# Performance work log

Hardware: AMD Instinct MI355X
Metric: run time of the kernel (lower is better)

## Reference

```python
import jax, jax.numpy as jnp
import numpy as np

B, LD = 256, 64
NO, LO = 10240, 32
NM, LM = 81920, 16
EO, EM = 81920, 327680
E, HID, H, Dh, V = 128, 256, 8, 16, 10000


def masked_mean(tokens, table):
    # tokens: [N, L] int; pad id = 0
    emb = table[tokens]                            # [N, L, E]
    mask = (tokens != 0)
    s = jnp.sum(emb * mask[..., None].astype(emb.dtype), axis=1)
    lens = jnp.maximum(jnp.sum(mask, axis=1), 1).astype(emb.dtype)
    return s / lens[:, None]


def segment_softmax(scores, seg, num_segments):
    # scores: [E, ...]; softmax over entries sharing seg id (PyG softmax)
    m = jax.ops.segment_max(scores, seg, num_segments=num_segments)
    e = jnp.exp(scores - m[seg])
    s = jax.ops.segment_sum(e, seg, num_segments=num_segments)
    return e / (s[seg] + 1e-16)


def gcn_conv(x, W, b, src, dst, n):
    # PyG GCNConv: normalize=True, add_self_loops=True
    xw = x @ W
    loops = jnp.arange(n, dtype=src.dtype)
    s2 = jnp.concatenate([src, loops])
    d2 = jnp.concatenate([dst, loops])
    deg = jax.ops.segment_sum(jnp.ones_like(d2, dtype=x.dtype), d2, num_segments=n)
    dinv = deg ** -0.5  # deg >= 1 due to self loops
    norm = dinv[s2] * dinv[d2]
    out = jax.ops.segment_sum(xw[s2] * norm[:, None], d2, num_segments=n)
    return out + b


def transformer_conv(x, Wq, bq, Wk, bk, Wv, bv, Wskip, bskip, src, dst, n):
    q = (x @ Wq + bq).reshape(n, H, Dh)
    k = (x @ Wk + bk).reshape(n, H, Dh)
    v = (x @ Wv + bv).reshape(n, H, Dh)
    score = jnp.sum(q[dst] * k[src], axis=-1) / jnp.sqrt(jnp.asarray(Dh, x.dtype))  # [E, H]
    alpha = segment_softmax(score, dst, n)
    agg = jax.ops.segment_sum(alpha[:, :, None] * v[src], dst, num_segments=n)  # [n, H, Dh]
    return agg.reshape(n, H * Dh) + x @ Wskip + bskip


def global_attention(x, Wg, bg, seg, num_segments):
    gate = x @ Wg + bg                              # [N, 1]
    a = segment_softmax(gate, seg, num_segments)
    return jax.ops.segment_sum(a * x, seg, num_segments=num_segments)


def setup_inputs():
    key = jax.random.key(0)
    ks = jax.random.split(key, 20)
    sc = lambda k, shape: jax.random.normal(k, shape, dtype=jnp.float32) * 0.05
    inp = {
        "desc_tokens": jax.random.randint(ks[0], (B, LD), 0, V, dtype=jnp.int32),
        "x_tokens": jax.random.randint(ks[1], (NO, LO), 0, V, dtype=jnp.int32),
        "mini_tokens": jax.random.randint(ks[2], (NM, LM), 0, V, dtype=jnp.int32),
        "src": jax.random.randint(ks[3], (EO,), 0, NO, dtype=jnp.int32),
        "dst": jax.random.randint(ks[4], (EO,), 0, NO, dtype=jnp.int32),
        "mini_src": jax.random.randint(ks[5], (EM,), 0, NM, dtype=jnp.int32),
        "mini_dst": jax.random.randint(ks[6], (EM,), 0, NM, dtype=jnp.int32),
        "mini_batch": (jnp.arange(NM, dtype=jnp.int32) // (NM // NO)),
        "node_batch": (jnp.arange(NO, dtype=jnp.int32) // (NO // B)),
        "desc_table": sc(ks[7], (V, E)),
        "code_table": sc(ks[8], (V, E)),
        "code_table2": sc(ks[9], (V, E)),
        "Wq": sc(ks[10], (E, H * Dh)), "bq": jnp.zeros((H * Dh,), jnp.float32),
        "Wk": sc(ks[11], (E, H * Dh)), "bk": jnp.zeros((H * Dh,), jnp.float32),
        "Wv": sc(ks[12], (E, H * Dh)), "bv": jnp.zeros((H * Dh,), jnp.float32),
        "Wskip": sc(ks[13], (E, H * Dh)), "bskip": jnp.zeros((H * Dh,), jnp.float32),
        "W2": sc(ks[14], (E, HID)), "b2": jnp.zeros((HID,), jnp.float32),
        "W3": sc(ks[15], (HID, E)), "b3": jnp.zeros((E,), jnp.float32),
        "Wg": sc(ks[16], (E, 1)), "bg": jnp.zeros((1,), jnp.float32),
    }
    return inp


def reference(desc_tokens, x_tokens, mini_tokens, src, dst, mini_src, mini_dst,
              mini_batch, node_batch, desc_table, code_table, code_table2,
              Wq, bq, Wk, bk, Wv, bv, Wskip, bskip, W2, b2, W3, b3, Wg, bg):
    # encode_desc: embedding + masked mean pool -> [B, E]
    h_n = masked_mean(desc_tokens, desc_table)
    # encode_code_graph
    stmt_emb = masked_mean(x_tokens, code_table2)          # [NO, E]
    mini_emb = masked_mean(mini_tokens, code_table)        # [NM, E]
    mini_hidden = transformer_conv(mini_emb, Wq, bq, Wk, bk, Wv, bv,
                                   Wskip, bskip, mini_src, mini_dst, NM)
    mini_fn = global_attention(mini_hidden, Wg, bg, mini_batch, NO)  # [NO, E]
    mini_fn = (mini_fn + stmt_emb) * 0.5
    h = jax.nn.relu(gcn_conv(mini_fn, W2, b2, src, dst, NO))
    final_stmt = gcn_conv(h, W3, b3, src, dst, NO)
    fn_repr = global_attention(final_stmt, Wg, bg, node_batch, B)    # [B, E]
    # cosine similarity (torch eps=1e-8 clamps each norm)
    na = jnp.maximum(jnp.linalg.norm(fn_repr, axis=-1), 1e-8)
    nb = jnp.maximum(jnp.linalg.norm(h_n, axis=-1), 1e-8)
    return jnp.sum(fn_repr * h_n, axis=-1) / (na * nb)
```

## Files before the change

### kernel.cpp

```cpp
#include <hip/hip_runtime.h>
#include <hip/hip_bf16.h>
#include <math.h>

#define BB   256
#define LDE  64
#define NO   10240
#define LO   32
#define NM   81920
#define LM   16
#define EO   81920
#define EM   327680
#define ED   128
#define HIDD 256
#define NH   8
#define DH   16
#define VV   10000

static inline int nblk(long long n, int b) { return (int)((n + b - 1) / b); }

typedef __attribute__((ext_vector_type(8))) short short8;
typedef __attribute__((ext_vector_type(4))) float f32x4;

static __device__ __forceinline__ unsigned short bf16_rne(float f) {
  unsigned u = __float_as_uint(f);
  return (unsigned short)((u + 0x7fffu + ((u >> 16) & 1u)) >> 16);
}
static __device__ __forceinline__ float bf16_to_f(unsigned short h) {
  return __uint_as_float(((unsigned)h) << 16);
}
static __device__ __forceinline__ float4 b4f(ushort4 h) {
  return make_float4(bf16_to_f(h.x), bf16_to_f(h.y), bf16_to_f(h.z), bf16_to_f(h.w));
}
static __device__ __forceinline__ ushort4 f4b(float4 v) {
  return make_ushort4(bf16_rne(v.x), bf16_rne(v.y), bf16_rne(v.z), bf16_rne(v.w));
}

static __device__ __forceinline__ void gl_lds16(const void* g, void* l) {
  __builtin_amdgcn_global_load_lds(
      (const __attribute__((address_space(1))) unsigned int*)g,
      (__attribute__((address_space(3))) unsigned int*)l, 16, 0, 0);
}

struct ConvArgs {
  const float *Wq, *Wk, *Wv, *Ws, *W2, *W3;
  const float *bq, *bk, *bv, *bs;
  short8* frag;
  float* bias512;
  const float* t1; unsigned short* o1;
  const float* t2; unsigned short* o2;
  int* hist;
};
#define TBLK (2 * VV * ED / 4 / 256)
#define ZBLK ((NM + NO) / 256)
__global__ void __launch_bounds__(256)
conv_all_k(ConvArgs A) {
  int b = blockIdx.x;
  if (b < 32) {
    int g = b * 256 + threadIdx.x;
    int lane = g & 63, f = g >> 6;
    int jl = f & 7, kb = (f >> 3) & 3, ch = f >> 5;
    int cf = ch * 8 + jl;
    int c = cf * 16 + (lane & 15);
    int k0 = kb * 32 + ((lane >> 4) << 3);
    const float* wp; int cm;
    if (c < 128)      { wp = A.Wq; cm = c; }
    else if (c < 384) { int u = c - 128, t = u & 7;
                        wp = (t < 4) ? A.Wk : A.Wv; cm = (u >> 3) * 4 + (t & 3); }
    else              { wp = A.Ws; cm = c - 384; }
    short8 h;
    #pragma unroll
    for (int j = 0; j < 8; ++j)
      h[j] = (short)bf16_rne(wp[(size_t)(k0 + j) * 128 + cm]);
    A.frag[g] = h;
  } else if (b < 64) {
    int g = (b - 32) * 256 + threadIdx.x;
    const float* wp; int M, dstbase, gg;
    if (g < 4096) { wp = A.W2; M = 256; dstbase = 8192;  gg = g; }
    else          { wp = A.W3; M = 128; dstbase = 12288; gg = g - 4096; }
    int lane = gg & 63, fid = gg >> 6;
    int nt = fid % (M / 16), kb = fid / (M / 16);
    int n = nt * 16 + (lane & 15);
    int k0 = kb * 32 + ((lane >> 4) << 3);
    short8 h;
    #pragma unroll
    for (int j = 0; j < 8; ++j)
      h[j] = (short)bf16_rne(wp[(size_t)(k0 + j) * M + n]);
    A.frag[dstbase + gg] = h;
  } else if (b < 64 + TBLK) {
    int q = (b - 64) * 256 + threadIdx.x;
    const int NT = VV * ED / 4;
    if (q < NT) {
      float4 v = *(const float4*)(A.t1 + (size_t)q * 4);
      *(ushort4*)(A.o1 + (size_t)q * 4) = f4b(v);
    } else if (q < 2 * NT) {
      int q2 = q - NT;
      float4 v = *(const float4*)(A.t2 + (size_t)q2 * 4);
      *(ushort4*)(A.o2 + (size_t)q2 * 4) = f4b(v);
    }
  } else if (b < 64 + TBLK + ZBLK) {
    int i = (b - 64 - TBLK) * 256 + threadIdx.x;
    if (i < NM + NO) A.hist[i] = 0;
  } else {
    for (int c = threadIdx.x; c < 512; c += 256) {
      float v;
      if (c < 128)      v = A.bq[c];
      else if (c < 384) { int u = c - 128, t = u & 7;
                          v = (t < 4) ? A.bk[(u >> 3) * 4 + t] : A.bv[(u >> 3) * 4 + (t & 3)]; }
      else              v = A.bs[c - 384];
      A.bias512[c] = v;
    }
  }
}

template<int L>
static __device__ __forceinline__ void embed_body_f(const int* __restrict__ tokens,
                                                    const float* __restrict__ table,
                                                    float* __restrict__ out, int blk) {
  const int r = threadIdx.x >> 5, lane = threadIdx.x & 31;
  const int n0 = blk * 8;
  __shared__ int toks[8][L];
  for (int i = threadIdx.x; i < 8 * L; i += 256)
    toks[i / L][i % L] = tokens[(size_t)n0 * L + i];
  __syncthreads();
  float4 acc = make_float4(0.f, 0.f, 0.f, 0.f);
  int cnt = 0;
  #pragma unroll
  for (int l = 0; l < L; ++l) {
    int t = toks[r][l];
    float4 v = *(const float4*)(table + (size_t)t * ED + lane * 4);
    float msk = (t != 0) ? 1.f : 0.f;
    cnt += (t != 0);
    acc.x = fmaf(msk, v.x, acc.x); acc.y = fmaf(msk, v.y, acc.y);
    acc.z = fmaf(msk, v.z, acc.z); acc.w = fmaf(msk, v.w, acc.w);
  }
  float inv = 1.f / (float)(cnt > 0 ? cnt : 1);
  acc.x *= inv; acc.y *= inv; acc.z *= inv; acc.w *= inv;
  *(float4*)(out + (size_t)(n0 + r) * ED + lane * 4) = acc;
}

template<int L>
static __device__ __forceinline__ void embed_body16(const int* __restrict__ tokens,
                                                    const unsigned short* __restrict__ table,
                                                    unsigned short* __restrict__ out, int blk) {
  const int r = threadIdx.x >> 4, lane = threadIdx.x & 15;
  const int n0 = blk * 16;
  __shared__ int toks[16][L];
  for (int i = threadIdx.x; i < 16 * L; i += 256)
    toks[i / L][i % L] = tokens[(size_t)n0 * L + i];
  __syncthreads();
  float acc[8] = {};
  int cnt = 0;
  #pragma unroll
  for (int l = 0; l < L; ++l) {
    int t = toks[r][l];
    short8 v = *(const short8*)(table + (size_t)t * ED + lane * 8);
    float msk = (t != 0) ? 1.f : 0.f;
    cnt += (t != 0);
    #pragma unroll
    for (int j = 0; j < 8; ++j)
      acc[j] = fmaf(msk, bf16_to_f((unsigned short)v[j]), acc[j]);
  }
  float inv = 1.f / (float)(cnt > 0 ? cnt : 1);
  short8 o;
  #pragma unroll
  for (int j = 0; j < 8; ++j) o[j] = (short)bf16_rne(acc[j] * inv);
  *(short8*)(out + (size_t)(n0 + r) * ED + lane * 8) = o;
}

__global__ void __launch_bounds__(256)
embed_all_k(const int* __restrict__ desc_tokens, const float* __restrict__ desc_table,
            float* __restrict__ h_n,
            const int* __restrict__ x_tokens, const unsigned short* __restrict__ ctab2,
            unsigned short* __restrict__ stmt,
            const int* __restrict__ mini_tokens, const unsigned short* __restrict__ ctab,
            unsigned short* __restrict__ miniE) {
  int b = blockIdx.x;
  if (b < BB / 8) embed_body_f<LDE>(desc_tokens, desc_table, h_n, b);
  else if (b < BB / 8 + NO / 16) embed_body16<LO>(x_tokens, ctab2, stmt, b - BB / 8);
  else embed_body16<LM>(mini_tokens, ctab, miniE, b - BB / 8 - NO / 16);
}

__global__ void __launch_bounds__(512)
qkvs_merged_k(const unsigned short* __restrict__ Ab, const short8* __restrict__ Wf,
              const float* __restrict__ bias512, unsigned short* __restrict__ out) {
  const int id = blockIdx.x;
  const int blk = (id & 7) * 80 + (id >> 3);
  const int n0 = blk * 128;
  const int tid = threadIdx.x;
  const int w = tid >> 6, lane = tid & 63;
  const int r = lane & 15, qd = lane >> 4;
  const int node = n0 + w * 16 + r;
  __shared__ short8 wlds[2048];
  __shared__ short8 elds[8 * 144];
  char* myl = (char*)elds + w * 2304;

  short8 a[4];
  #pragma unroll
  for (int kb = 0; kb < 4; ++kb)
    a[kb] = *(const short8*)(Ab + (size_t)node * ED + kb * 32 + qd * 8);

  for (int ch = 0; ch < 4; ++ch) {
    {
      const char* gs = (const char*)Wf + (size_t)ch * 32768
                     + (size_t)(w * 4) * 1024 + (size_t)lane * 16;
      char* ls = (char*)wlds + (w * 4) * 1024;
      #pragma unroll
      for (int t = 0; t < 4; ++t)
        gl_lds16(gs + t * 1024, ls + t * 1024);
    }
    __syncthreads();

    #pragma unroll
    for (int hf = 0; hf < 2; ++hf) {
      #pragma unroll
      for (int j4 = 0; j4 < 4; ++j4) {
        const int jl = hf * 4 + j4;
        f32x4 acc = (f32x4){0.f, 0.f, 0.f, 0.f};
        #pragma unroll
        for (int kb = 0; kb < 4; ++kb) {
          short8 wf = *(const short8*)((const char*)wlds
                        + ((size_t)((kb << 3) | jl) * 64 + lane) * 16);
          acc = __builtin_amdgcn_mfma_f32_16x16x32_bf16(wf, a[kb], acc, 0, 0, 0);
        }
        const int cf = ch * 8 + jl;
        const float4 bv = *(const float4*)(bias512 + cf * 16 + qd * 4);
        ushort4 o;
        o.x = bf16_rne(acc[0] + bv.x);
        o.y = bf16_rne(acc[1] + bv.y);
        o.z = bf16_rne(acc[2] + bv.z);
        o.w = bf16_rne(acc[3] + bv.w);
        *(ushort4*)(myl + r * 144 + j4 * 32 + qd * 8) = o;
      }
      #pragma unroll
      for (int t = 0; t < 2; ++t) {
        const int rr = t * 8 + (lane >> 3);
        short8 v = *(const short8*)(myl + rr * 144 + (lane & 7) * 16);
        *(short8*)(out + (size_t)(n0 + w * 16 + rr) * 512
                   + ch * 128 + hf * 64 + (lane & 7) * 8) = v;
      }
    }
    __syncthreads();
  }
}

template<bool RELU>
__global__ void __launch_bounds__(512)
mgemm_b_k(const unsigned short* __restrict__ Ab, const short8* __restrict__ Bh,
          const float* __restrict__ bias, unsigned short* __restrict__ C,
          int K, int M) {
  const int bn0 = blockIdx.x * 128;
  const int n0 = blockIdx.y * 128;
  const int tid = threadIdx.x;
  const int w = tid >> 6, lane = tid & 63;
  const int wm = (w & 3) * 2, wn = (w >> 2) * 4;
  const int r = lane & 15, qd = lane >> 4;
  const int NTm = M / 16;
  f32x4 acc[2][4];
  #pragma unroll
  for (int i = 0; i < 2; ++i)
    #pragma unroll
    for (int j = 0; j < 4; ++j) acc[i][j] = (f32x4){0.f, 0.f, 0.f, 0.f};
  const int kbn = K / 32;
  for (int kb = 0; kb < kbn; ++kb) {
    short8 bh[4];
    #pragma unroll
    for (int j = 0; j < 4; ++j)
      bh[j] = Bh[((size_t)kb * NTm + (bn0 >> 4) + wn + j) * 64 + lane];
    short8 a[2];
    #pragma unroll
    for (int i = 0; i < 2; ++i)
      a[i] = *(const short8*)(Ab + (size_t)(n0 + (wm + i) * 16 + r) * K + kb * 32 + qd * 8);
    #pragma unroll
    for (int i = 0; i < 2; ++i)
      #pragma unroll
      for (int j = 0; j < 4; ++j)
        acc[i][j] = __builtin_amdgcn_mfma_f32_16x16x32_bf16(bh[j], a[i], acc[i][j], 0, 0, 0);
  }
  #pragma unroll
  for (int i = 0; i < 2; ++i)
    #pragma unroll
    for (int j = 0; j < 4; ++j) {
      const int node = n0 + (wm + i) * 16 + r;
      const int colb = bn0 + (wn + j) * 16 + qd * 4;
      float4 bv = bias ? *(const float4*)(bias + colb) : make_float4(0.f, 0.f, 0.f, 0.f);
      float v0 = acc[i][j][0] + bv.x;
      float v1 = acc[i][j][1] + bv.y;
      float v2 = acc[i][j][2] + bv.z;
      float v3 = acc[i][j][3] + bv.w;
      if (RELU) {
        v0 = fmaxf(v0, 0.f); v1 = fmaxf(v1, 0.f);
        v2 = fmaxf(v2, 0.f); v3 = fmaxf(v3, 0.f);
      }
      ushort4 o = make_ushort4(bf16_rne(v0), bf16_rne(v1), bf16_rne(v2), bf16_rne(v3));
      *(ushort4*)(C + (size_t)node * M + colb) = o;
    }
}

__global__ void hist2_k(const int* __restrict__ dm, int* __restrict__ hm,
                        const int* __restrict__ dd, int* __restrict__ ho) {
  int e = blockIdx.x * 256 + threadIdx.x;
  if (e < EM) atomicAdd(&hm[dm[e]], 1);
  else { int e2 = e - EM; if (e2 < EO) atomicAdd(&ho[dd[e2]], 1); }
}
__global__ void chunk_sum_k(const int* __restrict__ hist, int* __restrict__ partials, int N) {
  __shared__ int sd[256];
  int i = blockIdx.x * 256 + threadIdx.x;
  sd[threadIdx.x] = (i < N) ? hist[i] : 0;
  __syncthreads();
  for (int s = 128; s > 0; s >>= 1) {
    if (threadIdx.x < s) sd[threadIdx.x] += sd[threadIdx.x + s];
    __syncthreads();
  }
  if (threadIdx.x == 0) partials[blockIdx.x] = sd[0];
}
__global__ void scan_partials2_k(int* __restrict__ p) {
  __shared__ int sd[512];
  int base = (blockIdx.x == 0) ? 0 : NM / 256;
  int B    = (blockIdx.x == 0) ? NM / 256 : NO / 256;
  int t = threadIdx.x;
  int v = (t < B) ? p[base + t] : 0;
  sd[t] = v; __syncthreads();
  for (int off = 1; off < 512; off <<= 1) {
    int a = (t >= off) ? sd[t - off] : 0;
    __syncthreads();
    sd[t] += a;
    __syncthreads();
  }
  if (t < B) p[base + t] = sd[t] - v;
}
__global__ void scan_final2_k(const int* __restrict__ hist, const int* __restrict__ partials,
                              int* __restrict__ offsm, int* __restrict__ curm,
                              int* __restrict__ offso, int* __restrict__ curo,
                              float* __restrict__ dinv) {
  __shared__ int sd[256];
  int i = blockIdx.x * 256 + threadIdx.x;
  int v = hist[i];
  sd[threadIdx.x] = v; __syncthreads();
  for (int off = 1; off < 256; off <<= 1) {
    int a = (threadIdx.x >= off) ? sd[threadIdx.x - off] : 0;
    __syncthreads();
    sd[threadIdx.x] += a;
    __syncthreads();
  }
  int excl = sd[threadIdx.x] - v + partials[blockIdx.x];
  if (i < NM) {
    offsm[i] = excl; curm[i] = excl;
    if (i == NM - 1) offsm[NM] = excl + v;
  } else {
    int i2 = i - NM;
    offso[i2] = excl; curo[i2] = excl;
    if (i2 == NO - 1) offso[NO] = excl + v;
    dinv[i2] = 1.f / sqrtf(1.f + (float)v);
  }
}
__global__ void scatter2_k(const int* __restrict__ sm, const int* __restrict__ dm,
                           int* __restrict__ cm, int* __restrict__ km,
                           const int* __restrict__ so, const int* __restrict__ dd,
                           int* __restrict__ co, int* __restrict__ ko) {
  int e = blockIdx.x * 256 + threadIdx.x;
  if (e < EM) {
    int pos = atomicAdd(&cm[dm[e]], 1);
    km[pos] = sm[e];
  } else {
    int e2 = e - EM;
    if (e2 < EO) {
      int pos = atomicAdd(&co[dd[e2]], 1);
      ko[pos] = so[e2];
    }
  }
}

__global__ void __launch_bounds__(128)
attn_fused_k(unsigned short* buf,
             const int* __restrict__ offs, const int* __restrict__ csr,
             const float* __restrict__ Wg, const float* __restrict__ bg,
             float* __restrict__ gateOut) {
  const int g = threadIdx.x >> 5, lane = threadIdx.x & 31;
  const int n = blockIdx.x * 4 + g;
  float4 q = b4f(*(const ushort4*)(buf + (size_t)n * 512 + lane * 4));
  int lo = offs[n], hi = offs[n + 1];
  float4 O = make_float4(0.f, 0.f, 0.f, 0.f);
  float m = -INFINITY, l = 0.f;
  for (int base = lo; base < hi; base += 4) {
    int rem = hi - base;
    int sidx[4];
    #pragma unroll
    for (int i = 0; i < 4; ++i) sidx[i] = (i < rem) ? csr[base + i] : 0;
    short8 kvr[4];
    #pragma unroll
    for (int i = 0; i < 4; ++i)
      kvr[i] = *(const short8*)(buf + (size_t)sidx[i] * 512 + 128 + lane * 8);
    #pragma unroll
    for (int i = 0; i < 4; ++i) {
      float4 kt = make_float4(bf16_to_f((unsigned short)kvr[i][0]),
                              bf16_to_f((unsigned short)kvr[i][1]),
                              bf16_to_f((unsigned short)kvr[i][2]),
                              bf16_to_f((unsigned short)kvr[i][3]));
      float4 vt = make_float4(bf16_to_f((unsigned short)kvr[i][4]),
                              bf16_to_f((unsigned short)kvr[i][5]),
                              bf16_to_f((unsigned short)kvr[i][6]),
                              bf16_to_f((unsigned short)kvr[i][7]));
      float p = q.x * kt.x + q.y * kt.y + q.z * kt.z + q.w * kt.w;
      p += __shfl_xor(p, 1, 64);
      p += __shfl_xor(p, 2, 64);
      float sc = (i < rem) ? p * 0.25f : -INFINITY;
      float mn = fmaxf(m, sc);
      float scale = __expf(m - mn);
      float pe = __expf(sc - mn);
      l = l * scale + pe;
      O.x = O.x * scale + pe * vt.x; O.y = O.y * scale + pe * vt.y;
      O.z = O.z * scale + pe * vt.z; O.w = O.w * scale + pe * vt.w;
      m = mn;
    }
  }
  float inv = 1.f / (l + 1e-16f);
  float4 sk = b4f(*(const ushort4*)(buf + (size_t)n * 512 + 384 + lane * 4));
  float4 out = make_float4(O.x * inv + sk.x, O.y * inv + sk.y,
                           O.z * inv + sk.z, O.w * inv + sk.w);
  *(ushort4*)(buf + (size_t)n * 512 + lane * 4) = f4b(out);
  float4 wg = *(const float4*)(Wg + lane * 4);
  float ps = out.x * wg.x + out.y * wg.y + out.z * wg.z + out.w * wg.w;
  #pragma unroll
  for (int o = 1; o <= 16; o <<= 1) ps += __shfl_xor(ps, o, 64);
  if (lane == 0) gateOut[n] = ps + bg[0];
}

__global__ void __launch_bounds__(256)
gcn_gather_b_k(const unsigned short* __restrict__ x, const float* __restrict__ dinv,
               const int* __restrict__ offs, const int* __restrict__ csr,
               const float* __restrict__ bias, unsigned short* __restrict__ out,
               const float* __restrict__ Wg, const float* __restrict__ bg,
               float* __restrict__ gateOut) {
  const int wv = threadIdx.x >> 6, lane = threadIdx.x & 63;
  const int half = lane >> 5, cl = lane & 31;
  const int n = blockIdx.x * 4 + wv;
  float di = dinv[n];
  float4 acc = make_float4(0.f, 0.f, 0.f, 0.f);
  if (half == 0) {
    float4 xs = b4f(*(const ushort4*)(x + (size_t)n * ED + cl * 4));
    float w0 = di * di;
    acc = make_float4(w0 * xs.x, w0 * xs.y, w0 * xs.z, w0 * xs.w);
  }
  int lo = offs[n], hi = offs[n + 1];
  for (int base = lo; base < hi; base += 8) {
    int sidx[4]; bool ok[4];
    #pragma unroll
    for (int i = 0; i < 4; ++i) {
      int e = base + 2 * i + half;
      ok[i] = e < hi;
      sidx[i] = ok[i] ? csr[e] : 0;
    }
    float dw[4];
    #pragma unroll
    for (int i = 0; i < 4; ++i) dw[i] = ok[i] ? di * dinv[sidx[i]] : 0.f;
    ushort4 vr[4];
    #pragma unroll
    for (int i = 0; i < 4; ++i)
      vr[i] = *(const ushort4*)(x + (size_t)sidx[i] * ED + cl * 4);
    #pragma unroll
    for (int i = 0; i < 4; ++i) {
      float4 v = b4f(vr[i]);
      acc.x = fmaf(dw[i], v.x, acc.x); acc.y = fmaf(dw[i], v.y, acc.y);
      acc.z = fmaf(dw[i], v.z, acc.z); acc.w = fmaf(dw[i], v.w, acc.w);
    }
  }
  acc.x += __shfl_xor(acc.x, 32, 64); acc.y += __shfl_xor(acc.y, 32, 64);
  acc.z += __shfl_xor(acc.z, 32, 64); acc.w += __shfl_xor(acc.w, 32, 64);
  if (bias) {
    float4 b4 = *(const float4*)(bias + cl * 4);
    acc.x += b4.x; acc.y += b4.y; acc.z += b4.z; acc.w += b4.w;
  }
  if (half == 0)
    *(ushort4*)(out + (size_t)n * ED + cl * 4) = f4b(acc);
  if (gateOut) {
    float4 wg = *(const float4*)(Wg + cl * 4);
    float ps = acc.x * wg.x + acc.y * wg.y + acc.z * wg.z + acc.w * wg.w;
    #pragma unroll
    for (int o = 1; o <= 16; o <<= 1) ps += __shfl_xor(ps, o, 64);
    if (lane == 0) gateOut[n] = ps + bg[0];
  }
}

static __device__ __forceinline__ int lower_bound_d(const int* a, int n, int key) {
  int lo = 0, hi = n;
  while (lo < hi) { int mid = (lo + hi) >> 1; if (a[mid] < key) lo = mid + 1; else hi = mid; }
  return lo;
}
__global__ void __launch_bounds__(128)
gattn_comb_b_k(const unsigned short* __restrict__ xv, const float* __restrict__ gate,
               const int* __restrict__ seg, int Ntot,
               const unsigned short* __restrict__ other, unsigned short* __restrict__ out) {
  const int g = threadIdx.x >> 5, lane = threadIdx.x & 31;
  const int n = blockIdx.x * 4 + g;
  __shared__ int sh[4][2];
  if (lane == 0) {
    sh[g][0] = lower_bound_d(seg, Ntot, n);
    sh[g][1] = lower_bound_d(seg, Ntot, n + 1);
  }
  __syncthreads();
  int lo = sh[g][0], hi = sh[g][1];
  float m = -INFINITY;
  for (int j = lo; j < hi; ++j) m = fmaxf(m, gate[j]);
  float ssum = 0.f;
  for (int j = lo; j < hi; ++j) ssum += __expf(gate[j] - m);
  float inv = 1.f / (ssum + 1e-16f);
  float4 acc = make_float4(0.f, 0.f, 0.f, 0.f);
  for (int j = lo; j < hi; ++j) {
    float a = __expf(gate[j] - m) * inv;
    float4 v = b4f(*(const ushort4*)(xv + (size_t)j * 512 + lane * 4));
    acc.x = fmaf(a, v.x, acc.x); acc.y = fmaf(a, v.y, acc.y);
    acc.z = fmaf(a, v.z, acc.z); acc.w = fmaf(a, v.w, acc.w);
  }
  float4 o4 = b4f(*(const ushort4*)(other + (size_t)n * ED + lane * 4));
  acc.x = (acc.x + o4.x) * 0.5f; acc.y = (acc.y + o4.y) * 0.5f;
  acc.z = (acc.z + o4.z) * 0.5f; acc.w = (acc.w + o4.w) * 0.5f;
  *(ushort4*)(out + (size_t)n * ED + lane * 4) = f4b(acc);
}

__global__ void __launch_bounds__(128)
gattn_cos_k(const unsigned short* __restrict__ x, const float* __restrict__ gate,
            const int* __restrict__ seg, int Ntot,
            const float* __restrict__ hn, float* __restrict__ outp) {
  const int g = threadIdx.x >> 5, lane = threadIdx.x & 31;
  const int n = blockIdx.x * 4 + g;
  __shared__ int sh[4][2];
  if (lane == 0) {
    sh[g][0] = lower_bound_d(seg, Ntot, n);
    sh[g][1] = lower_bound_d(seg, Ntot, n + 1);
  }
  __syncthreads();
  int lo = sh[g][0], hi = sh[g][1];
  float m = -INFINITY;
  for (int j = lo; j < hi; ++j) m = fmaxf(m, gate[j]);
  float ssum = 0.f;
  for (int j = lo; j < hi; ++j) ssum += __expf(gate[j] - m);
  float inv = 1.f / (ssum + 1e-16f);
  float4 acc = make_float4(0.f, 0.f, 0.f, 0.f);
  for (int j = lo; j < hi; ++j) {
    float a = __expf(gate[j] - m) * inv;
    float4 v = b4f(*(const ushort4*)(x + (size_t)j * ED + lane * 4));
    acc.x = fmaf(a, v.x, acc.x); acc.y = fmaf(a, v.y, acc.y);
    acc.z = fmaf(a, v.z, acc.z); acc.w = fmaf(a, v.w, acc.w);
  }
  float4 hv = *(const float4*)(hn + (size_t)n * ED + lane * 4);
  float dot = acc.x * hv.x + acc.y * hv.y + acc.z * hv.z + acc.w * hv.w;
  float na  = acc.x * acc.x + acc.y * acc.y + acc.z * acc.z + acc.w * acc.w;
  float nb  = hv.x * hv.x + hv.y * hv.y + hv.z * hv.z + hv.w * hv.w;
  #pragma unroll
  for (int o = 1; o <= 16; o <<= 1) {
    dot += __shfl_xor(dot, o, 64);
    na  += __shfl_xor(na,  o, 64);
    nb  += __shfl_xor(nb,  o, 64);
  }
  if (lane == 0)
    outp[n] = dot / (fmaxf(sqrtf(na), 1e-8f) * fmaxf(sqrtf(nb), 1e-8f));
}

constexpr size_t OFF_HN    = 0;
constexpr size_t OFF_STMT  = OFF_HN    + (size_t)BB * ED;
constexpr size_t OFF_A     = OFF_STMT  + (size_t)NO * ED;
constexpr size_t OFF_CT    = OFF_A     + (size_t)NM * ED;
constexpr size_t OFF_QKVS  = OFF_CT    + (size_t)VV * ED;
constexpr size_t T0        = OFF_QKVS  + (size_t)NM * 256;
constexpr size_t OFF_GATE  = T0;
constexpr size_t OFF_GATE2 = OFF_GATE  + (size_t)NM;
constexpr size_t OFF_DINV  = OFF_GATE2 + (size_t)NO;
constexpr size_t OFF_HISTM = OFF_DINV  + (size_t)NO;
constexpr size_t OFF_HISTO = OFF_HISTM + (size_t)NM;
constexpr size_t OFF_OFFSM = OFF_HISTO + (size_t)NO;
constexpr size_t OFF_CURM  = OFF_OFFSM + (size_t)NM + 1;
constexpr size_t OFF_CSRM  = OFF_CURM  + (size_t)NM;
constexpr size_t OFF_OFFSO = OFF_CSRM  + (size_t)EM;
constexpr size_t OFF_CURO  = OFF_OFFSO + (size_t)NO + 1;
constexpr size_t OFF_CSRO  = OFF_CURO  + (size_t)NO;
constexpr size_t OFF_PART  = OFF_CSRO  + (size_t)EO;
constexpr size_t OFF_B512  = OFF_PART  + 512;
constexpr size_t OFF_WFHI  = OFF_B512  + 512;
constexpr size_t OFF_MFN   = OFF_A;
constexpr size_t OFF_AGG   = OFF_MFN   + (size_t)NO * ED;
constexpr size_t OFF_H     = OFF_AGG   + (size_t)NO * ED;
constexpr size_t OFF_T     = OFF_H     + (size_t)NO * HIDD;
constexpr size_t OFF_FIN   = OFF_T     + (size_t)NO * ED;

extern "C" void kernel_launch(void* const* d_in, const int* in_sizes, int n_in,
                              void* d_out, int out_size, void* d_ws, size_t ws_size,
                              hipStream_t stream) {
  const int* desc_tokens = (const int*)d_in[0];
  const int* x_tokens    = (const int*)d_in[1];
  const int* mini_tokens = (const int*)d_in[2];
  const int* src         = (const int*)d_in[3];
  const int* dst         = (const int*)d_in[4];
  const int* mini_src    = (const int*)d_in[5];
  const int* mini_dst    = (const int*)d_in[6];
  const int* mini_batch  = (const int*)d_in[7];
  const int* node_batch  = (const int*)d_in[8];
  const float* desc_table  = (const float*)d_in[9];
  const float* code_table  = (const float*)d_in[10];
  const float* code_table2 = (const float*)d_in[11];
  const float* Wq = (const float*)d_in[12]; const float* bq = (const float*)d_in[13];
  const float* Wk = (const float*)d_in[14]; const float* bk = (const float*)d_in[15];
  const float* Wv = (const float*)d_in[16]; const float* bv = (const float*)d_in[17];
  const float* Wskip = (const float*)d_in[18]; const float* bskip = (const float*)d_in[19];
  const float* W2 = (const float*)d_in[20]; const float* b2 = (const float*)d_in[21];
  const float* W3 = (const float*)d_in[22]; const float* b3 = (const float*)d_in[23];
  const float* Wg = (const float*)d_in[24]; const float* bg = (const float*)d_in[25];

  float* ws = (float*)d_ws;
  float* h_n   = ws + OFF_HN;
  unsigned short* stmt_b  = (unsigned short*)(ws + OFF_STMT);
  unsigned short* miniE_b = (unsigned short*)(ws + OFF_A);
  unsigned short* ctab_b  = (unsigned short*)(ws + OFF_CT);
  unsigned short* ctab2_b = ctab_b + (size_t)VV * ED;
  unsigned short* qkvs_b  = (unsigned short*)(ws + OFF_QKVS);
  float* gate  = ws + OFF_GATE;
  float* gate2 = ws + OFF_GATE2;
  float* dinv  = ws + OFF_DINV;
  int* histm = (int*)(ws + OFF_HISTM);
  int* histo = (int*)(ws + OFF_HISTO);
  int* offsm = (int*)(ws + OFF_OFFSM);
  int* curm  = (int*)(ws + OFF_CURM);
  int* csrm  = (int*)(ws + OFF_CSRM);
  int* offso = (int*)(ws + OFF_OFFSO);
  int* curo  = (int*)(ws + OFF_CURO);
  int* csro  = (int*)(ws + OFF_CSRO);
  int* part  = (int*)(ws + OFF_PART);
  float* bias512 = ws + OFF_B512;
  short8* wfrag = (short8*)(ws + OFF_WFHI);
  unsigned short* mini_fn_b = (unsigned short*)(ws + OFF_MFN);
  unsigned short* aggb_b    = (unsigned short*)(ws + OFF_AGG);
  unsigned short* hbuf_b    = (unsigned short*)(ws + OFF_H);
  unsigned short* tbuf_b    = (unsigned short*)(ws + OFF_T);
  unsigned short* finalS_b  = (unsigned short*)(ws + OFF_FIN);
  float* outp    = (float*)d_out;

  ConvArgs ca;
  ca.Wq = Wq; ca.Wk = Wk; ca.Wv = Wv; ca.Ws = Wskip; ca.W2 = W2; ca.W3 = W3;
  ca.bq = bq; ca.bk = bk; ca.bv = bv; ca.bs = bskip;
  ca.frag = wfrag; ca.bias512 = bias512;
  ca.t1 = code_table;  ca.o1 = ctab_b;
  ca.t2 = code_table2; ca.o2 = ctab2_b;
  ca.hist = histm;
  conv_all_k<<<64 + TBLK + ZBLK + 1, 256, 0, stream>>>(ca);

  hist2_k<<<nblk(EM + EO, 256), 256, 0, stream>>>(mini_dst, histm, dst, histo);
  chunk_sum_k<<<(NM + NO) / 256, 256, 0, stream>>>(histm, part, NM + NO);
  scan_partials2_k<<<2, 512, 0, stream>>>(part);
  scan_final2_k<<<(NM + NO) / 256, 256, 0, stream>>>(histm, part, offsm, curm,
                                                     offso, curo, dinv);
  scatter2_k<<<nblk(EM + EO, 256), 256, 0, stream>>>(mini_src, mini_dst, curm, csrm,
                                                     src, dst, curo, csro);

  embed_all_k<<<BB / 8 + NO / 16 + NM / 16, 256, 0, stream>>>(
      desc_tokens, desc_table, h_n, x_tokens, ctab2_b, stmt_b,
      mini_tokens, ctab_b, miniE_b);

  qkvs_merged_k<<<NM / 128, 512, 0, stream>>>(miniE_b, wfrag, bias512, qkvs_b);

  attn_fused_k<<<NM / 4, 128, 0, stream>>>(qkvs_b, offsm, csrm, Wg, bg, gate);

  gattn_comb_b_k<<<NO / 4, 128, 0, stream>>>(qkvs_b, gate, mini_batch, NM,
                                             stmt_b, mini_fn_b);

  gcn_gather_b_k<<<NO / 4, 256, 0, stream>>>(mini_fn_b, dinv, offso, csro, nullptr,
                                             aggb_b, nullptr, nullptr, nullptr);
  { dim3 g(HIDD / 128, NO / 128);
    mgemm_b_k<true><<<g, 512, 0, stream>>>(aggb_b, wfrag + 8192, b2, hbuf_b, ED, HIDD); }

  { dim3 g(1, NO / 128);
    mgemm_b_k<false><<<g, 512, 0, stream>>>(hbuf_b, wfrag + 12288, nullptr, tbuf_b, HIDD, ED); }
  gcn_gather_b_k<<<NO / 4, 256, 0, stream>>>(tbuf_b, dinv, offso, csro, b3, finalS_b,
                                             Wg, bg, gate2);

  gattn_cos_k<<<BB / 4, 128, 0, stream>>>(finalS_b, gate2, node_batch, NO, h_n, outp);
}
```

Measured before the change: 328.7 us.

## Fuse edge histogram into embed kernel, restructure QKV epilogue and attention softmax

Folds the destination-degree histogram atomics into the embedding kernel as extra blocks, removing one launch and letting the atomics overlap the gather-heavy embedding work. The QKV GEMM now computes all eight output tiles before one barrier, then reuses the weight LDS buffer with an XOR swizzle to stage full 128-column rows for wider stores. The attention loop processes four edges per online-softmax update with a single rescale, and hoists the skip and gate loads to the start. This adds register pressure and an extra barrier in the GEMM in exchange for fewer launches and fewer exponentials.

```diff
diff --git a/kernel.cpp b/kernel.cpp
--- a/kernel.cpp
+++ b/kernel.cpp
@@ -167,17 +167,94 @@
   *(short8*)(out + (size_t)(n0 + r) * ED + lane * 8) = o;
 }
 
+#define HBLK ((EM + EO) / 256)
 __global__ void __launch_bounds__(256)
 embed_all_k(const int* __restrict__ desc_tokens, const float* __restrict__ desc_table,
             float* __restrict__ h_n,
             const int* __restrict__ x_tokens, const unsigned short* __restrict__ ctab2,
             unsigned short* __restrict__ stmt,
             const int* __restrict__ mini_tokens, const unsigned short* __restrict__ ctab,
-            unsigned short* __restrict__ miniE) {
+            unsigned short* __restrict__ miniE,
+            const int* __restrict__ mini_dst, const int* __restrict__ dst,
+            int* __restrict__ histm, int* __restrict__ histo) {
   int b = blockIdx.x;
-  if (b < BB / 8) embed_body_f<LDE>(desc_tokens, desc_table, h_n, b);
-  else if (b < BB / 8 + NO / 16) embed_body16<LO>(x_tokens, ctab2, stmt, b - BB / 8);
-  else embed_body16<LM>(mini_tokens, ctab, miniE, b - BB / 8 - NO / 16);
+  if (b < HBLK) {
+    int e = b * 256 + threadIdx.x;
+    if (e < EM) atomicAdd(&histm[mini_dst[e]], 1);
+    else        atomicAdd(&histo[dst[e - EM]], 1);
+  }
+  else if (b < HBLK + BB / 8) embed_body_f<LDE>(desc_tokens, desc_table, h_n, b - HBLK);
+  else if (b < HBLK + BB / 8 + NO / 16)
+    embed_body16<LO>(x_tokens, ctab2, stmt, b - HBLK - BB / 8);
+  else embed_body16<LM>(mini_tokens, ctab, miniE, b - HBLK - BB / 8 - NO / 16);
+}
+
+__global__ void chunk_sum_k(const int* __restrict__ hist, int* __restrict__ partials, int N) {
+  __shared__ int sd[256];
+  int i = blockIdx.x * 256 + threadIdx.x;
+  sd[threadIdx.x] = (i < N) ? hist[i] : 0;
+  __syncthreads();
+  for (int s = 128; s > 0; s >>= 1) {
+    if (threadIdx.x < s) sd[threadIdx.x] += sd[threadIdx.x + s];
+    __syncthreads();
+  }
+  if (threadIdx.x == 0) partials[blockIdx.x] = sd[0];
+}
+__global__ void scan_partials2_k(int* __restrict__ p) {
+  __shared__ int sd[512];
+  int base = (blockIdx.x == 0) ? 0 : NM / 256;
+  int B    = (blockIdx.x == 0) ? NM / 256 : NO / 256;
+  int t = threadIdx.x;
+  int v = (t < B) ? p[base + t] : 0;
+  sd[t] = v; __syncthreads();
+  for (int off = 1; off < 512; off <<= 1) {
+    int a = (t >= off) ? sd[t - off] : 0;
+    __syncthreads();
+    sd[t] += a;
+    __syncthreads();
+  }
+  if (t < B) p[base + t] = sd[t] - v;
+}
+__global__ void scan_final2_k(const int* __restrict__ hist, const int* __restrict__ partials,
+                              int* __restrict__ offsm, int* __restrict__ curm,
+                              int* __restrict__ offso, int* __restrict__ curo,
+                              float* __restrict__ dinv) {
+  __shared__ int sd[256];
+  int i = blockIdx.x * 256 + threadIdx.x;
+  int v = hist[i];
+  sd[threadIdx.x] = v; __syncthreads();
+  for (int off = 1; off < 256; off <<= 1) {
+    int a = (threadIdx.x >= off) ? sd[threadIdx.x - off] : 0;
+    __syncthreads();
+    sd[threadIdx.x] += a;
+    __syncthreads();
+  }
+  int excl = sd[threadIdx.x] - v + partials[blockIdx.x];
+  if (i < NM) {
+    offsm[i] = excl; curm[i] = excl;
+    if (i == NM - 1) offsm[NM] = excl + v;
+  } else {
+    int i2 = i - NM;
+    offso[i2] = excl; curo[i2] = excl;
+    if (i2 == NO - 1) offso[NO] = excl + v;
+    dinv[i2] = 1.f / sqrtf(1.f + (float)v);
+  }
+}
+__global__ void scatter2_k(const int* __restrict__ sm, const int* __restrict__ dm,
+                           int* __restrict__ cm, int* __restrict__ km,
+                           const int* __restrict__ so, const int* __restrict__ dd,
+                           int* __restrict__ co, int* __restrict__ ko) {
+  int e = blockIdx.x * 256 + threadIdx.x;
+  if (e < EM) {
+    int pos = atomicAdd(&cm[dm[e]], 1);
+    km[pos] = sm[e];
+  } else {
+    int e2 = e - EM;
+    if (e2 < EO) {
+      int pos = atomicAdd(&co[dd[e2]], 1);
+      ko[pos] = so[e2];
+    }
+  }
 }
 
 __global__ void __launch_bounds__(512)
@@ -191,8 +268,7 @@
   const int r = lane & 15, qd = lane >> 4;
   const int node = n0 + w * 16 + r;
   __shared__ short8 wlds[2048];
-  __shared__ short8 elds[8 * 144];
-  char* myl = (char*)elds + w * 2304;
+  char* myl = (char*)wlds + w * 4096;
 
   short8 a[4];
   #pragma unroll
@@ -210,34 +286,35 @@
     }
     __syncthreads();
 
-    #pragma unroll
-    for (int hf = 0; hf < 2; ++hf) {
+    f32x4 acc[8];
+    #pragma unroll
+    for (int jl = 0; jl < 8; ++jl) acc[jl] = (f32x4){0.f, 0.f, 0.f, 0.f};
+    #pragma unroll
+    for (int kb = 0; kb < 4; ++kb)
       #pragma unroll
-      for (int j4 = 0; j4 < 4; ++j4) {
-        const int jl = hf * 4 + j4;
-        f32x4 acc = (f32x4){0.f, 0.f, 0.f, 0.f};
-        #pragma unroll
-        for (int kb = 0; kb < 4; ++kb) {
-          short8 wf = *(const short8*)((const char*)wlds
-                        + ((size_t)((kb << 3) | jl) * 64 + lane) * 16);
-          acc = __builtin_amdgcn_mfma_f32_16x16x32_bf16(wf, a[kb], acc, 0, 0, 0);
-        }
-        const int cf = ch * 8 + jl;
-        const float4 bv = *(const float4*)(bias512 + cf * 16 + qd * 4);
-        ushort4 o;
-        o.x = bf16_rne(acc[0] + bv.x);
-        o.y = bf16_rne(acc[1] + bv.y);
-        o.z = bf16_rne(acc[2] + bv.z);
-        o.w = bf16_rne(acc[3] + bv.w);
-        *(ushort4*)(myl + r * 144 + j4 * 32 + qd * 8) = o;
+      for (int jl = 0; jl < 8; ++jl) {
+        short8 wf = *(const short8*)((const char*)wlds
+                      + ((size_t)((kb << 3) | jl) * 64 + lane) * 16);
+        acc[jl] = __builtin_amdgcn_mfma_f32_16x16x32_bf16(wf, a[kb], acc[jl], 0, 0, 0);
       }
-      #pragma unroll
-      for (int t = 0; t < 2; ++t) {
-        const int rr = t * 8 + (lane >> 3);
-        short8 v = *(const short8*)(myl + rr * 144 + (lane & 7) * 16);
-        *(short8*)(out + (size_t)(n0 + w * 16 + rr) * 512
-                   + ch * 128 + hf * 64 + (lane & 7) * 8) = v;
-      }
+    __syncthreads();
+
+    #pragma unroll
+    for (int jl = 0; jl < 8; ++jl) {
+      const int cf = ch * 8 + jl;
+      const float4 bv = *(const float4*)(bias512 + cf * 16 + qd * 4);
+      ushort4 o;
+      o.x = bf16_rne(acc[jl][0] + bv.x);
+      o.y = bf16_rne(acc[jl][1] + bv.y);
+      o.z = bf16_rne(acc[jl][2] + bv.z);
+      o.w = bf16_rne(acc[jl][3] + bv.w);
+      *(ushort4*)(myl + r * 256 + ((jl * 32) ^ ((r & 7) << 5)) + qd * 8) = o;
+    }
+    #pragma unroll
+    for (int t = 0; t < 4; ++t) {
+      const int rr = t * 4 + qd;
+      short8 v = *(const short8*)(myl + rr * 256 + (((lane & 15) * 16) ^ ((rr & 7) << 5)));
+      *(short8*)(out + (size_t)(n0 + w * 16 + rr) * 512 + ch * 128 + (lane & 15) * 8) = v;
     }
     __syncthreads();
   }
@@ -296,80 +373,6 @@
     }
 }
 
-__global__ void hist2_k(const int* __restrict__ dm, int* __restrict__ hm,
-                        const int* __restrict__ dd, int* __restrict__ ho) {
-  int e = blockIdx.x * 256 + threadIdx.x;
-  if (e < EM) atomicAdd(&hm[dm[e]], 1);
-  else { int e2 = e - EM; if (e2 < EO) atomicAdd(&ho[dd[e2]], 1); }
-}
-__global__ void chunk_sum_k(const int* __restrict__ hist, int* __restrict__ partials, int N) {
-  __shared__ int sd[256];
-  int i = blockIdx.x * 256 + threadIdx.x;
-  sd[threadIdx.x] = (i < N) ? hist[i] : 0;
-  __syncthreads();
-  for (int s = 128; s > 0; s >>= 1) {
-    if (threadIdx.x < s) sd[threadIdx.x] += sd[threadIdx.x + s];
-    __syncthreads();
-  }
-  if (threadIdx.x == 0) partials[blockIdx.x] = sd[0];
-}
-__global__ void scan_partials2_k(int* __restrict__ p) {
-  __shared__ int sd[512];
-  int base = (blockIdx.x == 0) ? 0 : NM / 256;
-  int B    = (blockIdx.x == 0) ? NM / 256 : NO / 256;
-  int t = threadIdx.x;
-  int v = (t < B) ? p[base + t] : 0;
-  sd[t] = v; __syncthreads();
-  for (int off = 1; off < 512; off <<= 1) {
-    int a = (t >= off) ? sd[t - off] : 0;
-    __syncthreads();
-    sd[t] += a;
-    __syncthreads();
-  }
-  if (t < B) p[base + t] = sd[t] - v;
-}
-__global__ void scan_final2_k(const int* __restrict__ hist, const int* __restrict__ partials,
-                              int* __restrict__ offsm, int* __restrict__ curm,
-                              int* __restrict__ offso, int* __restrict__ curo,
-                              float* __restrict__ dinv) {
-  __shared__ int sd[256];
-  int i = blockIdx.x * 256 + threadIdx.x;
-  int v = hist[i];
-  sd[threadIdx.x] = v; __syncthreads();
-  for (int off = 1; off < 256; off <<= 1) {
-    int a = (threadIdx.x >= off) ? sd[threadIdx.x - off] : 0;
-    __syncthreads();
-    sd[threadIdx.x] += a;
-    __syncthreads();
-  }
-  int excl = sd[threadIdx.x] - v + partials[blockIdx.x];
-  if (i < NM) {
-    offsm[i] = excl; curm[i] = excl;
-    if (i == NM - 1) offsm[NM] = excl + v;
-  } else {
-    int i2 = i - NM;
-    offso[i2] = excl; curo[i2] = excl;
-    if (i2 == NO - 1) offso[NO] = excl + v;
-    dinv[i2] = 1.f / sqrtf(1.f + (float)v);
-  }
-}
-__global__ void scatter2_k(const int* __restrict__ sm, const int* __restrict__ dm,
-                           int* __restrict__ cm, int* __restrict__ km,
-                           const int* __restrict__ so, const int* __restrict__ dd,
-                           int* __restrict__ co, int* __restrict__ ko) {
-  int e = blockIdx.x * 256 + threadIdx.x;
-  if (e < EM) {
-    int pos = atomicAdd(&cm[dm[e]], 1);
-    km[pos] = sm[e];
-  } else {
-    int e2 = e - EM;
-    if (e2 < EO) {
-      int pos = atomicAdd(&co[dd[e2]], 1);
-      ko[pos] = so[e2];
-    }
-  }
-}
-
 __global__ void __launch_bounds__(128)
 attn_fused_k(unsigned short* buf,
              const int* __restrict__ offs, const int* __restrict__ csr,
@@ -378,6 +381,8 @@
   const int g = threadIdx.x >> 5, lane = threadIdx.x & 31;
   const int n = blockIdx.x * 4 + g;
   float4 q = b4f(*(const ushort4*)(buf + (size_t)n * 512 + lane * 4));
+  float4 sk = b4f(*(const ushort4*)(buf + (size_t)n * 512 + 384 + lane * 4));
+  float4 wg = *(const float4*)(Wg + lane * 4);
   int lo = offs[n], hi = offs[n + 1];
   float4 O = make_float4(0.f, 0.f, 0.f, 0.f);
   float m = -INFINITY, l = 0.f;
@@ -390,35 +395,39 @@
     #pragma unroll
     for (int i = 0; i < 4; ++i)
       kvr[i] = *(const short8*)(buf + (size_t)sidx[i] * 512 + 128 + lane * 8);
+    float sc[4]; float4 vt[4];
     #pragma unroll
     for (int i = 0; i < 4; ++i) {
       float4 kt = make_float4(bf16_to_f((unsigned short)kvr[i][0]),
                               bf16_to_f((unsigned short)kvr[i][1]),
                               bf16_to_f((unsigned short)kvr[i][2]),
                               bf16_to_f((unsigned short)kvr[i][3]));
-      float4 vt = make_float4(bf16_to_f((unsigned short)kvr[i][4]),
-                              bf16_to_f((unsigned short)kvr[i][5]),
-                              bf16_to_f((unsigned short)kvr[i][6]),
-                              bf16_to_f((unsigned short)kvr[i][7]));
+      vt[i] = make_float4(bf16_to_f((unsigned short)kvr[i][4]),
+                          bf16_to_f((unsigned short)kvr[i][5]),
+                          bf16_to_f((unsigned short)kvr[i][6]),
+                          bf16_to_f((unsigned short)kvr[i][7]));
       float p = q.x * kt.x + q.y * kt.y + q.z * kt.z + q.w * kt.w;
       p += __shfl_xor(p, 1, 64);
       p += __shfl_xor(p, 2, 64);
-      float sc = (i < rem) ? p * 0.25f : -INFINITY;
-      float mn = fmaxf(m, sc);
-      float scale = __expf(m - mn);
-      float pe = __expf(sc - mn);
-      l = l * scale + pe;
-      O.x = O.x * scale + pe * vt.x; O.y = O.y * scale + pe * vt.y;
-      O.z = O.z * scale + pe * vt.z; O.w = O.w * scale + pe * vt.w;
-      m = mn;
-    }
+      sc[i] = (i < rem) ? p * 0.25f : -INFINITY;
+    }
+    float mt = fmaxf(fmaxf(sc[0], sc[1]), fmaxf(sc[2], sc[3]));
+    float mn = fmaxf(m, mt);
+    float scale = __expf(m - mn);
+    float pe[4];
+    #pragma unroll
+    for (int i = 0; i < 4; ++i) pe[i] = __expf(sc[i] - mn);
+    l = l * scale + ((pe[0] + pe[1]) + (pe[2] + pe[3]));
+    O.x = fmaf(pe[3], vt[3].x, fmaf(pe[2], vt[2].x, fmaf(pe[1], vt[1].x, fmaf(pe[0], vt[0].x, O.x * scale))));
+    O.y = fmaf(pe[3], vt[3].y, fmaf(pe[2], vt[2].y, fmaf(pe[1], vt[1].y, fmaf(pe[0], vt[0].y, O.y * scale))));
+    O.z = fmaf(pe[3], vt[3].z, fmaf(pe[2], vt[2].z, fmaf(pe[1], vt[1].z, fmaf(pe[0], vt[0].z, O.z * scale))));
+    O.w = fmaf(pe[3], vt[3].w, fmaf(pe[2], vt[2].w, fmaf(pe[1], vt[1].w, fmaf(pe[0], vt[0].w, O.w * scale))));
+    m = mn;
   }
   float inv = 1.f / (l + 1e-16f);
-  float4 sk = b4f(*(const ushort4*)(buf + (size_t)n * 512 + 384 + lane * 4));
   float4 out = make_float4(O.x * inv + sk.x, O.y * inv + sk.y,
                            O.z * inv + sk.z, O.w * inv + sk.w);
   *(ushort4*)(buf + (size_t)n * 512 + lane * 4) = f4b(out);
-  float4 wg = *(const float4*)(Wg + lane * 4);
   float ps = out.x * wg.x + out.y * wg.y + out.z * wg.z + out.w * wg.w;
   #pragma unroll
   for (int o = 1; o <= 16; o <<= 1) ps += __shfl_xor(ps, o, 64);
@@ -642,7 +651,10 @@
   ca.hist = histm;
   conv_all_k<<<64 + TBLK + ZBLK + 1, 256, 0, stream>>>(ca);
 
-  hist2_k<<<nblk(EM + EO, 256), 256, 0, stream>>>(mini_dst, histm, dst, histo);
+  embed_all_k<<<HBLK + BB / 8 + NO / 16 + NM / 16, 256, 0, stream>>>(
+      desc_tokens, desc_table, h_n, x_tokens, ctab2_b, stmt_b,
+      mini_tokens, ctab_b, miniE_b, mini_dst, dst, histm, histo);
+
   chunk_sum_k<<<(NM + NO) / 256, 256, 0, stream>>>(histm, part, NM + NO);
   scan_partials2_k<<<2, 512, 0, stream>>>(part);
   scan_final2_k<<<(NM + NO) / 256, 256, 0, stream>>>(histm, part, offsm, curm,
@@ -650,10 +662,6 @@
   scatter2_k<<<nblk(EM + EO, 256), 256, 0, stream>>>(mini_src, mini_dst, curm, csrm,
                                                      src, dst, curo, csro);
 
-  embed_all_k<<<BB / 8 + NO / 16 + NM / 16, 256, 0, stream>>>(
-      desc_tokens, desc_table, h_n, x_tokens, ctab2_b, stmt_b,
-      mini_tokens, ctab_b, miniE_b);
-
   qkvs_merged_k<<<NM / 128, 512, 0, stream>>>(miniE_b, wfrag, bias512, qkvs_b);
 
   attn_fused_k<<<NM / 4, 128, 0, stream>>>(qkvs_b, offsm, csrm, Wg, bg, gate);
```

Result: no change. 329.8 us (+0.3%).
